# Performance work log

Measured on AMD Instinct MI355X. Metric: run time of the kernel, lower is better.

The kernel has to match this reference:

```python
import jax, jax.numpy as jnp
import numpy as np

B, C, H, W = 4, 256, 32, 32
N_HEADS, N_GROUPS = 8, 4
HEAD_C = C // N_HEADS            # 32
GROUP_C = C // N_GROUPS          # 64
GROUP_HEADS = N_HEADS // N_GROUPS  # 2
OFFSET_RANGE_FACTOR = 4.0
SCALE = HEAD_C ** -0.5
EPS = 1e-5


def grid_sample(img, grid):
    """Bilinear grid_sample, align_corners=True, zeros padding.
    img: (N, Ch, Hi, Wi); grid: (N, Hg, Wg, 2) with (x, y) in [-1, 1]."""
    N, Ch, Hi, Wi = img.shape
    x = (grid[..., 0] + 1.0) * 0.5 * (Wi - 1)
    y = (grid[..., 1] + 1.0) * 0.5 * (Hi - 1)
    x0 = jnp.floor(x); y0 = jnp.floor(y)
    x1 = x0 + 1.0; y1 = y0 + 1.0
    wx1 = x - x0; wx0 = 1.0 - wx1
    wy1 = y - y0; wy0 = 1.0 - wy1
    img_flat = img.reshape(N, Ch, Hi * Wi)

    def corner(xi, yi, w):
        valid = (xi >= 0) & (xi <= Wi - 1) & (yi >= 0) & (yi <= Hi - 1)
        xc = jnp.clip(xi, 0, Wi - 1).astype(jnp.int32)
        yc = jnp.clip(yi, 0, Hi - 1).astype(jnp.int32)
        idx = yc * Wi + xc  # (N, Hg, Wg)
        vals = jax.vmap(lambda im, ix: im[:, ix])(img_flat, idx)  # (N, Ch, Hg, Wg)
        return vals * (w * valid)[:, None, :, :]

    return (corner(x0, y0, wx0 * wy0) + corner(x1, y0, wx1 * wy0)
            + corner(x0, y1, wx0 * wy1) + corner(x1, y1, wx1 * wy1))


def setup_inputs() -> dict:
    key = jax.random.key(0)
    ks = jax.random.split(key, 12)
    s = C ** -0.5
    return {
        "q_feat": jax.random.normal(ks[0], (B, C, H, W), jnp.float32),
        "kv_feat": jax.random.normal(ks[1], (B, C, H, W), jnp.float32),
        "Wq": jax.random.normal(ks[2], (C, C), jnp.float32) * s,
        "bq": jnp.zeros((C,), jnp.float32),
        "Wk": jax.random.normal(ks[3], (C, C), jnp.float32) * s,
        "bk": jnp.zeros((C,), jnp.float32),
        "Wv": jax.random.normal(ks[4], (C, C), jnp.float32) * s,
        "bv": jnp.zeros((C,), jnp.float32),
        "Wo": jax.random.normal(ks[5], (C, C), jnp.float32) * s,
        "bo": jnp.zeros((C,), jnp.float32),
        "off_dw_w": jax.random.normal(ks[6], (GROUP_C, 1, 3, 3), jnp.float32) / 3.0,
        "off_dw_b": jnp.zeros((GROUP_C,), jnp.float32),
        "off_ln_w": jnp.ones((GROUP_C,), jnp.float32),
        "off_ln_b": jnp.zeros((GROUP_C,), jnp.float32),
        "off_pw_w": jax.random.normal(ks[7], (2, GROUP_C), jnp.float32) * GROUP_C ** -0.5,
        "rpe_table": jax.random.normal(ks[8], (N_HEADS, 2 * H - 1, 2 * W - 1), jnp.float32) * 0.01,
    }


def reference(q_feat, kv_feat, Wq, bq, Wk, bk, Wv, bv, Wo, bo,
              off_dw_w, off_dw_b, off_ln_w, off_ln_b, off_pw_w, rpe_table):
    Bg = B * N_GROUPS
    n = H * W
    # q projection (1x1 conv)
    q = jnp.einsum('oi,bihw->bohw', Wq, q_feat) + bq[:, None, None]
    # offset network on grouped q
    q_off = q.reshape(Bg, GROUP_C, H, W)
    x = jax.lax.conv_general_dilated(q_off, off_dw_w, (1, 1), ((1, 1), (1, 1)),
                                     feature_group_count=GROUP_C,
                                     dimension_numbers=('NCHW', 'OIHW', 'NCHW'))
    x = x + off_dw_b[:, None, None]
    mu = x.mean(1, keepdims=True)
    var = x.var(1, keepdims=True)
    x = (x - mu) / jnp.sqrt(var + EPS) * off_ln_w[:, None, None] + off_ln_b[:, None, None]
    x = jax.nn.gelu(x, approximate=False)
    offset = jnp.einsum('oc,bchw->bohw', off_pw_w, x)  # (Bg, 2, H, W), (y, x)
    off_range = jnp.array([1.0 / (H - 1), 1.0 / (W - 1)], jnp.float32).reshape(1, 2, 1, 1)
    offset = jnp.tanh(offset) * off_range * OFFSET_RANGE_FACTOR
    offset = offset.transpose(0, 2, 3, 1)  # (Bg, H, W, 2)
    # reference points in [-1, 1]
    ref_y = (jnp.linspace(0.5, H - 0.5, H) / (H - 1.0)) * 2.0 - 1.0
    ref_x = (jnp.linspace(0.5, W - 0.5, W) / (W - 1.0)) * 2.0 - 1.0
    ref = jnp.stack(jnp.meshgrid(ref_y, ref_x, indexing='ij'), -1)  # (H, W, 2)
    pos = offset + ref[None]  # (Bg, H, W, 2), (y, x), no clamp (offset_range_factor >= 0)
    # deformable sampling of kv features
    kv_g = kv_feat.reshape(Bg, GROUP_C, H, W)
    x_sampled = grid_sample(kv_g, pos[..., ::-1]).reshape(B, C, n)
    k = jnp.einsum('oi,bin->bon', Wk, x_sampled) + bk[:, None]
    v = jnp.einsum('oi,bin->bon', Wv, x_sampled) + bv[:, None]
    qf = q.reshape(B, N_HEADS, HEAD_C, n)
    kf = k.reshape(B, N_HEADS, HEAD_C, n)
    vf = v.reshape(B, N_HEADS, HEAD_C, n)
    attn = jnp.einsum('bhcm,bhcn->bhmn', qf, kf) * SCALE
    # relative-position bias via bilinear sampling of rpe table
    gy = (jnp.arange(H, dtype=jnp.float32) / (H - 1.0)) * 2.0 - 1.0
    gx = (jnp.arange(W, dtype=jnp.float32) / (W - 1.0)) * 2.0 - 1.0
    q_grid = jnp.stack(jnp.meshgrid(gy, gx, indexing='ij'), -1).reshape(n, 2)
    pos_flat = pos.reshape(Bg, n, 2)
    disp = (q_grid[None, :, None, :] - pos_flat[:, None, :, :]) * 0.5  # (Bg, m, n, 2)
    rpe = jnp.broadcast_to(
        rpe_table.reshape(1, N_GROUPS, GROUP_HEADS, 2 * H - 1, 2 * W - 1),
        (B, N_GROUPS, GROUP_HEADS, 2 * H - 1, 2 * W - 1)
    ).reshape(Bg, GROUP_HEADS, 2 * H - 1, 2 * W - 1)
    bias = grid_sample(rpe, disp[..., ::-1])  # (Bg, GROUP_HEADS, m, n)
    attn = attn + bias.reshape(B, N_HEADS, n, n)
    attn = jax.nn.softmax(attn, axis=-1)
    out = jnp.einsum('bhmn,bhcn->bhcm', attn, vf).reshape(B, C, H, W)
    out = jnp.einsum('oi,bihw->bohw', Wo, out) + bo[:, None, None]
    return out
```

## Files before the change

### kernel.cpp

```cpp
#include <hip/hip_runtime.h>
#include <hip/hip_bf16.h>
#include <math.h>

#define BB 4
#define CC 256
#define HH 32
#define WW 32
#define NPIX 1024
#define NHEADS 8
#define NGROUPS 4
#define HEADC 32
#define GROUPC 64
#define BG 16
#define RPE_N 3969
#define SCALE_QK 0.17677669529663687f
#define LN_EPS 1e-5f

#define W_Q   0
#define W_POS 1048576
#define W_XS  1081344
#define W_KT  2129920
#define W_VV  2654208
#define W_AO  3178496

using frag  = __attribute__((ext_vector_type(8))) short;
using f32x4 = __attribute__((ext_vector_type(4))) float;

struct InPtrs { const void* p[16]; };

__device__ __forceinline__ float tof(float x){ return x; }
__device__ __forceinline__ float tof(__hip_bfloat16 x){ return __bfloat162float(x); }
__device__ __forceinline__ short bfs(float v) {
  __hip_bfloat16 h = __float2bfloat16(v);
  return *(short*)&h;
}
__device__ __forceinline__ bool is_f32(const void* lnw) {
  return *(const unsigned int*)lnw == 0x3F800000u;
}
__device__ __forceinline__ float ldm(const void* p, size_t i, bool f32m) {
  return f32m ? ((const float*)p)[i] : __bfloat162float(((const __hip_bfloat16*)p)[i]);
}

template<int TM>
__device__ __forceinline__ void gemm_body(const void* xsrc, bool xf32,
    const void* wraw, bool wf32, int b, int o0, int mb,
    short* Bs, f32x4* acc) {
  const int tid = threadIdx.x;
  const int wave = tid >> 6, lane = tid & 63, quad = lane >> 4, l15 = lane & 15;
  const int og = wave & 3, mh = wave >> 2;
  const int MS = TM >> 5;
  const int NE = TM >> 4;

  size_t gbase[NE];
  int lbase[NE];
  #pragma unroll
  for (int it = 0; it < NE; ++it) {
    int i = tid + 512 * it;
    int mm = i & (TM - 1), kk = i / TM;
    gbase[it] = ((size_t)(b * CC + kk)) * NPIX + mb + mm;
    lbase[it] = mm * 72 + ((((kk >> 3) ^ (mm & 3))) << 4) + (kk & 7);
  }

  float v[NE];
  #pragma unroll
  for (int it = 0; it < NE; ++it)
    v[it] = xf32 ? ((const float*)xsrc)[gbase[it]]
                 : __bfloat162float(((const __hip_bfloat16*)xsrc)[gbase[it]]);

  for (int s = 0; s < 8; ++s) {
    short* buf = Bs + (s & 1) * (TM * 72);
    #pragma unroll
    for (int it = 0; it < NE; ++it) {
      __hip_bfloat16 h = __float2bfloat16(v[it]);
      buf[lbase[it]] = *(short*)&h;
      buf[lbase[it] + 8] = bfs(v[it] - __bfloat162float(h));
    }
    if (s < 7) {
      size_t koff = (size_t)(s + 1) * 32 * NPIX;
      #pragma unroll
      for (int it = 0; it < NE; ++it)
        v[it] = xf32 ? ((const float*)xsrc)[gbase[it] + koff]
                     : __bfloat162float(((const __hip_bfloat16*)xsrc)[gbase[it] + koff]);
    }
    const int k0 = s * 32;
    size_t wofs = (size_t)(o0 + og * 16 + l15) * CC + k0 + quad * 8;
    float wv[8];
    if (wf32) {
      float4 wa = *(const float4*)((const float*)wraw + wofs);
      float4 wb = *(const float4*)((const float*)wraw + wofs + 4);
      wv[0]=wa.x; wv[1]=wa.y; wv[2]=wa.z; wv[3]=wa.w;
      wv[4]=wb.x; wv[5]=wb.y; wv[6]=wb.z; wv[7]=wb.w;
    } else {
      const __hip_bfloat16* wp = (const __hip_bfloat16*)wraw + wofs;
      #pragma unroll
      for (int j = 0; j < 8; ++j) wv[j] = __bfloat162float(wp[j]);
    }
    frag wh, wl;
    #pragma unroll
    for (int j = 0; j < 8; ++j) {
      __hip_bfloat16 h = __float2bfloat16(wv[j]);
      wh[j] = *(short*)&h;
      wl[j] = bfs(wv[j] - __bfloat162float(h));
    }
    __syncthreads();
    #pragma unroll
    for (int ms = 0; ms < MS; ++ms) {
      int ml = mh * (TM >> 1) + ms * 16 + l15;
      const short* bp = buf + ml * 72 + ((quad ^ (ml & 3)) << 4);
      frag bh = *(const frag*)bp;
      frag bl = *(const frag*)(bp + 8);
      acc[ms] = __builtin_amdgcn_mfma_f32_16x16x32_bf16(wh, bh, acc[ms], 0, 0, 0);
      acc[ms] = __builtin_amdgcn_mfma_f32_16x16x32_bf16(wh, bl, acc[ms], 0, 0, 0);
      acc[ms] = __builtin_amdgcn_mfma_f32_16x16x32_bf16(wl, bh, acc[ms], 0, 0, 0);
    }
  }
}

__global__ __launch_bounds__(512)
void qproj_kernel(InPtrs ip, float* __restrict__ q) {
  __shared__ __align__(16) short Bs[2 * 32 * 72];
  bool f32m = is_f32(ip.p[12]);
  int mb = blockIdx.x * 32, o0 = blockIdx.y * 64, b = blockIdx.z;
  int tid = threadIdx.x;
  int wave = tid >> 6, lane = tid & 63, quad = lane >> 4, l15 = lane & 15;
  f32x4 acc[1] = {{0.f,0.f,0.f,0.f}};
  gemm_body<32>(ip.p[0], f32m, ip.p[2], f32m, b, o0, mb, Bs, acc);
  int og = wave & 3, mh = wave >> 2;
  int od = o0 + og * 16 + quad * 4;
  float bv[4];
  #pragma unroll
  for (int r = 0; r < 4; ++r) bv[r] = ldm(ip.p[3], od + r, f32m);
  int m = mb + mh * 16 + l15;
  #pragma unroll
  for (int r = 0; r < 4; ++r)
    q[(size_t)(b * CC + od + r) * NPIX + m] = acc[0][r] + bv[r];
}

__global__ __launch_bounds__(512)
void kvproj_kernel(InPtrs ip, const float* __restrict__ xs,
                   __hip_bfloat16* __restrict__ kT, __hip_bfloat16* __restrict__ vbf) {
  __shared__ __align__(16) char arena[2 * 64 * 72 * 2];
  bool f32m = is_f32(ip.p[12]);
  int mt = blockIdx.x, ot = blockIdx.y, b = blockIdx.z;
  int mb = mt * 64;
  bool isV = (ot >= 4);
  int o0 = (ot & 3) * 64;
  const void* wraw = isV ? ip.p[6] : ip.p[4];
  const void* braw = isV ? ip.p[7] : ip.p[5];
  int tid = threadIdx.x;
  int wave = tid >> 6, lane = tid & 63, quad = lane >> 4, l15 = lane & 15;
  f32x4 acc[2] = {{0.f,0.f,0.f,0.f},{0.f,0.f,0.f,0.f}};
  gemm_body<64>(xs, true, wraw, f32m, b, o0, mb, (short*)arena, acc);
  int og = wave & 3, mh = wave >> 2;
  int od = o0 + og * 16 + quad * 4;
  float bv[4];
  #pragma unroll
  for (int r = 0; r < 4; ++r) bv[r] = ldm(braw, od + r, f32m);
  if (isV) {
    #pragma unroll
    for (int ms = 0; ms < 2; ++ms) {
      int m = mb + mh * 32 + ms * 16 + l15;
      #pragma unroll
      for (int r = 0; r < 4; ++r)
        vbf[(size_t)(b * CC + od + r) * NPIX + m] = __float2bfloat16(acc[ms][r] + bv[r]);
    }
  } else {
    __syncthreads();
    float* Ds = (float*)arena;
    #pragma unroll
    for (int ms = 0; ms < 2; ++ms) {
      int ml = mh * 32 + ms * 16 + l15;
      #pragma unroll
      for (int r = 0; r < 4; ++r)
        Ds[(og * 16 + quad * 4 + r) * 65 + ml] = acc[ms][r] + bv[r];
    }
    __syncthreads();
    int ot4 = ot & 3;
    {
      int q2 = tid;
      int m = q2 >> 3, cc = q2 & 7;
      __hip_bfloat16 t8[8];
      #pragma unroll
      for (int j = 0; j < 8; ++j)
        t8[j] = __float2bfloat16(Ds[(cc * 8 + j) * 65 + m]);
      int h = ot4 * 2 + (cc >> 2);
      size_t addr = ((size_t)(b * NHEADS + h) * NPIX + mb + m) * HEADC + (cc & 3) * 8;
      *(uint4*)((short*)kT + addr) = *(const uint4*)t8;
    }
  }
}

__global__ __launch_bounds__(512)
void oproj_kernel(InPtrs ip, const float* __restrict__ ao, void* __restrict__ out) {
  __shared__ __align__(16) short Bs[2 * 32 * 72];
  bool f32m = is_f32(ip.p[12]);
  int mb = blockIdx.x * 32, o0 = blockIdx.y * 64, b = blockIdx.z;
  int tid = threadIdx.x;
  int wave = tid >> 6, lane = tid & 63, quad = lane >> 4, l15 = lane & 15;
  f32x4 acc[1] = {{0.f,0.f,0.f,0.f}};
  gemm_body<32>(ao, true, ip.p[8], f32m, b, o0, mb, Bs, acc);
  int og = wave & 3, mh = wave >> 2;
  int od = o0 + og * 16 + quad * 4;
  float bv[4];
  #pragma unroll
  for (int r = 0; r < 4; ++r) bv[r] = ldm(ip.p[9], od + r, f32m);
  int m = mb + mh * 16 + l15;
  #pragma unroll
  for (int r = 0; r < 4; ++r) {
    float val = acc[0][r] + bv[r];
    size_t idx = (size_t)(b * CC + od + r) * NPIX + m;
    if (f32m) ((float*)out)[idx] = val;
    else      ((__hip_bfloat16*)out)[idx] = __float2bfloat16(val);
  }
}

template<typename T>
__device__ __forceinline__ float tap4(const T* __restrict__ img,
                                      int x0, int y0,
                                      float wx0, float wx1, float wy0, float wy1) {
  bool xv0 = (x0 >= 0) & (x0 < WW);
  bool xv1 = (x0 >= -1) & (x0 < WW - 1);
  bool yv0 = (y0 >= 0) & (y0 < HH);
  bool yv1 = (y0 >= -1) & (y0 < HH - 1);
  float acc = 0.0f;
  if (xv0 & yv0) acc += wx0 * wy0 * tof(img[y0 * WW + x0]);
  if (xv1 & yv0) acc += wx1 * wy0 * tof(img[y0 * WW + x0 + 1]);
  if (xv0 & yv1) acc += wx0 * wy1 * tof(img[(y0 + 1) * WW + x0]);
  if (xv1 & yv1) acc += wx1 * wy1 * tof(img[(y0 + 1) * WW + x0 + 1]);
  return acc;
}

__global__ __launch_bounds__(512)
void offsample_kernel(InPtrs ip, const float* __restrict__ q,
                      float* __restrict__ pos, float* __restrict__ xs) {
  __shared__ float qs[128][65];
  __shared__ float posl[2][64];
  bool f32m = is_f32(ip.p[12]);
  int blk = blockIdx.x;
  int hh2 = blk & 15, bg = blk >> 4;
  int b = bg >> 2, g = bg & 3;
  int tid = threadIdx.x;
  const float* qg = q + (size_t)(b * CC + g * GROUPC) * NPIX;
  #pragma unroll
  for (int k = 0; k < 16; ++k) {
    int idx = tid + 512 * k;
    int ww = idx & 31, c = (idx >> 5) & 63, r3 = idx >> 11;
    int yy = hh2 * 2 - 1 + r3;
    float v = (yy >= 0 && yy < HH) ? qg[(size_t)c * NPIX + yy * WW + ww] : 0.0f;
    qs[r3 * 32 + ww][c] = v;
  }
  __syncthreads();
  {
    int wave = tid >> 6, c = tid & 63;
    int lr = wave >> 2, w4 = wave & 3;
    float wdw[9];
    #pragma unroll
    for (int j = 0; j < 9; ++j) wdw[j] = ldm(ip.p[10], c * 9 + j, f32m);
    float bdw = ldm(ip.p[11], c, f32m);
    float lnw = ldm(ip.p[12], c, f32m), lnb = ldm(ip.p[13], c, f32m);
    float pwy = ldm(ip.p[14], c, f32m), pwx = ldm(ip.p[14], GROUPC + c, f32m);

    for (int p8 = 0; p8 < 8; ++p8) {
      int ww = w4 * 8 + p8;
      float x = bdw;
      #pragma unroll
      for (int dy = 0; dy < 3; ++dy)
        #pragma unroll
        for (int dx = 0; dx < 3; ++dx) {
          int xx = ww + dx - 1;
          if (xx >= 0 && xx < WW) x += wdw[dy * 3 + dx] * qs[(lr + dy) * 32 + xx][c];
        }
      float s = x, s2 = x * x;
      #pragma unroll
      for (int off = 32; off > 0; off >>= 1) {
        s  += __shfl_xor(s,  off);
        s2 += __shfl_xor(s2, off);
      }
      float mu  = s * (1.0f / 64.0f);
      float var = s2 * (1.0f / 64.0f) - mu * mu;
      float xn = (x - mu) * (1.0f / sqrtf(var + LN_EPS)) * lnw + lnb;
      float ge = 0.5f * xn * (1.0f + erff(xn * 0.70710678118654752f));
      float oy = pwy * ge, ox = pwx * ge;
      #pragma unroll
      for (int off = 32; off > 0; off >>= 1) {
        oy += __shfl_xor(oy, off);
        ox += __shfl_xor(ox, off);
      }
      if (c == 0) {
        int hh = hh2 * 2 + lr;
        float fy = tanhf(oy) * (4.0f / 31.0f);
        float fx = tanhf(ox) * (4.0f / 31.0f);
        float ry = ((0.5f + (float)hh) / 31.0f) * 2.0f - 1.0f;
        float rx = ((0.5f + (float)ww) / 31.0f) * 2.0f - 1.0f;
        float py = fy + ry, px = fx + rx;
        int m = hh * 32 + ww;
        pos[((size_t)bg * NPIX + m) * 2 + 0] = py;
        pos[((size_t)bg * NPIX + m) * 2 + 1] = px;
        posl[lr][ww * 2 + 0] = py;
        posl[lr][ww * 2 + 1] = px;
      }
    }
  }
  __syncthreads();
  #pragma unroll
  for (int k = 0; k < 8; ++k) {
    int s = tid + 512 * k;
    int ww = s & 31, lr = (s >> 5) & 1, c = s >> 6;
    float py = posl[lr][ww * 2 + 0], px = posl[lr][ww * 2 + 1];
    float xi = (px + 1.0f) * 15.5f, yi = (py + 1.0f) * 15.5f;
    float x0f = floorf(xi), y0f = floorf(yi);
    float wx1 = xi - x0f, wx0 = 1.0f - wx1;
    float wy1 = yi - y0f, wy0 = 1.0f - wy1;
    int x0 = (int)x0f, y0 = (int)y0f;
    size_t img_off = (size_t)(b * CC + g * GROUPC + c) * NPIX;
    float acc;
    if (f32m) acc = tap4((const float*)ip.p[1] + img_off, x0, y0, wx0, wx1, wy0, wy1);
    else      acc = tap4((const __hip_bfloat16*)ip.p[1] + img_off, x0, y0, wx0, wx1, wy0, wy1);
    xs[img_off + (hh2 * 2 + lr) * 32 + ww] = acc;
  }
}

__global__ __launch_bounds__(512)
void attn_mfma_kernel(InPtrs ip, const float* __restrict__ q,
                      const __hip_bfloat16* __restrict__ kT,
                      const __hip_bfloat16* __restrict__ vbf,
                      const float* __restrict__ pos, float* __restrict__ ao) {
  __shared__ __align__(16) __hip_bfloat16 Pl[16][1032];
  __shared__ float rpes[RPE_N];
  __shared__ __align__(16) __hip_bfloat16 qA[4][16][40];
  __shared__ float redmax[8 * 16];
  __shared__ float redsum[8 * 16];

  bool f32m = is_f32(ip.p[12]);
  int bh = blockIdx.x;
  int b = bh >> 3, h = bh & 7;
  int m0base = blockIdx.y * 64;
  int tid = threadIdx.x;
  int bg = b * 4 + (h >> 1);

  size_t slice = (size_t)(b * CC + h * HEADC) * NPIX;
  const short* kTb = (const short*)kT + (size_t)bh * NPIX * HEADC;
  const short* vb = (const short*)vbf + slice;
  const float* qb = q + slice;
  const float* posb = pos + (size_t)bg * NPIX * 2;

  for (int i = tid; i < RPE_N; i += 512)
    rpes[i] = ldm(ip.p[15], (size_t)h * RPE_N + i, f32m);
  #pragma unroll
  for (int e = 0; e < 4; ++e) {
    int idx = tid + 512 * e;
    int t = idx >> 9, j = idx & 511;
    int r = j & 15, c = j >> 4;
    qA[t][r][c] = __float2bfloat16(qb[(size_t)c * NPIX + m0base + t * 16 + r] * SCALE_QK);
  }
  __syncthreads();

  int wave = tid >> 6, lane = tid & 63;
  int quad = lane >> 4, l15 = lane & 15;
  int nbase = wave * 128;

  for (int t = 0; t < 4; ++t) {
    int m0 = m0base + t * 16;
    if (t) __syncthreads();

    frag aq = *(const frag*)&qA[t][l15][quad * 8];
    float qgy = (float)(m0 >> 5) * (2.0f / 31.0f) - 1.0f;
    float ybase = 31.0f + 15.5f * qgy;
    float qgx0 = (float)(m0 & 31) * (2.0f / 31.0f) - 1.0f;
    float xbase0 = 31.0f + 15.5f * qgx0;

    float sreg[8][4];
    #pragma unroll
    for (int t8 = 0; t8 < 8; ++t8) {
      int n = nbase + t8 * 16 + l15;
      frag bk = *(const frag*)(kTb + (size_t)n * HEADC + quad * 8);
      f32x4 d = __builtin_amdgcn_mfma_f32_16x16x32_bf16(aq, bk, (f32x4){0.f,0.f,0.f,0.f}, 0, 0, 0);
      float2 pp = *(const float2*)(posb + 2 * n);
      float yi = ybase - 15.5f * pp.x;
      float y0f = floorf(yi);
      int y0 = (int)y0f;
      float wy1 = yi - y0f, wy0 = 1.0f - wy1;
      bool yv0 = (y0 >= 0) & (y0 < 63);
      bool yv1 = (y0 >= -1) & (y0 < 62);
      int row0 = y0 * 63;
      float xi0 = xbase0 - 15.5f * pp.y;
      float x0f = floorf(xi0);
      int x0 = (int)x0f;
      float wx1 = xi0 - x0f, wx0 = 1.0f - wx1;
      float u[5];
      #pragma unroll
      for (int jj = 0; jj < 5; ++jj) {
        int xj = x0 + quad * 4 + jj;
        bool xv = (xj >= 0) & (xj < 63);
        int a = row0 + xj;
        int a0c = min(max(a, 0), RPE_N - 1);
        int a1c = min(max(a + 63, 0), RPE_N - 1);
        float t0 = (yv0 & xv) ? rpes[a0c] : 0.0f;
        float t1 = (yv1 & xv) ? rpes[a1c] : 0.0f;
        u[jj] = wy0 * t0 + wy1 * t1;
      }
      #pragma unroll
      for (int reg = 0; reg < 4; ++reg)
        sreg[t8][reg] = d[reg] + wx0 * u[reg] + wx1 * u[reg + 1];
    }

    float ps[4], pm[4];
    #pragma unroll
    for (int reg = 0; reg < 4; ++reg) {
      float m = sreg[0][reg];
      #pragma unroll
      for (int t8 = 1; t8 < 8; ++t8) m = fmaxf(m, sreg[t8][reg]);
      m = fmaxf(m, __shfl_xor(m, 1));
      m = fmaxf(m, __shfl_xor(m, 2));
      m = fmaxf(m, __shfl_xor(m, 4));
      m = fmaxf(m, __shfl_xor(m, 8));
      pm[reg] = m;
      ps[reg] = 0.0f;
    }
    #pragma unroll
    for (int t8 = 0; t8 < 8; ++t8) {
      int n = nbase + t8 * 16 + l15;
      #pragma unroll
      for (int reg = 0; reg < 4; ++reg) {
        float p = __expf(sreg[t8][reg] - pm[reg]);
        Pl[quad * 4 + reg][n] = __float2bfloat16(p);
        ps[reg] += p;
      }
    }
    #pragma unroll
    for (int reg = 0; reg < 4; ++reg) {
      ps[reg] += __shfl_xor(ps[reg], 1);
      ps[reg] += __shfl_xor(ps[reg], 2);
      ps[reg] += __shfl_xor(ps[reg], 4);
      ps[reg] += __shfl_xor(ps[reg], 8);
    }
    if (l15 == 0) {
      #pragma unroll
      for (int reg = 0; reg < 4; ++reg) {
        redmax[wave * 16 + quad * 4 + reg] = pm[reg];
        redsum[wave * 16 + quad * 4 + reg] = ps[reg];
      }
    }

    f32x4 acc0 = {0.f,0.f,0.f,0.f}, acc1 = {0.f,0.f,0.f,0.f};
    #pragma unroll
    for (int ks = 0; ks < 4; ++ks) {
      int koff = nbase + ks * 32 + quad * 8;
      frag ap = *(const frag*)&Pl[l15][koff];
      frag bv0 = *(const frag*)(vb + (size_t)l15 * NPIX + koff);
      frag bv1 = *(const frag*)(vb + (size_t)(16 + l15) * NPIX + koff);
      acc0 = __builtin_amdgcn_mfma_f32_16x16x32_bf16(ap, bv0, acc0, 0, 0, 0);
      acc1 = __builtin_amdgcn_mfma_f32_16x16x32_bf16(ap, bv1, acc1, 0, 0, 0);
    }
    __syncthreads();

    float* part = (float*)&Pl[0][0];
    {
      int e0 = (0 * 16 + l15) * 16 + quad * 4;
      int e1 = (1 * 16 + l15) * 16 + quad * 4;
      #pragma unroll
      for (int reg = 0; reg < 4; ++reg) {
        part[wave * 512 + e0 + reg] = acc0[reg];
        part[wave * 512 + e1 + reg] = acc1[reg];
      }
    }
    __syncthreads();

    {
      int c = tid >> 4, r = tid & 15;
      float M = -1e30f;
      #pragma unroll
      for (int w2 = 0; w2 < 8; ++w2) M = fmaxf(M, redmax[w2 * 16 + r]);
      float num = 0.0f, den = 0.0f;
      #pragma unroll
      for (int w2 = 0; w2 < 8; ++w2) {
        float sc = __expf(redmax[w2 * 16 + r] - M);
        num += part[w2 * 512 + tid] * sc;
        den += redsum[w2 * 16 + r] * sc;
      }
      ao[slice + (size_t)c * NPIX + m0 + r] = num / den;
    }
  }
}

extern "C" void kernel_launch(void* const* d_in, const int* in_sizes, int n_in,
                              void* d_out, int out_size, void* d_ws, size_t ws_size,
                              hipStream_t stream) {
  float* ws  = (float*)d_ws;
  float* q   = ws + W_Q;
  float* pos = ws + W_POS;
  float* xs  = ws + W_XS;
  __hip_bfloat16* kT  = (__hip_bfloat16*)(ws + W_KT);
  __hip_bfloat16* vbf = (__hip_bfloat16*)(ws + W_VV);
  float* ao  = ws + W_AO;

  InPtrs ip;
  for (int i = 0; i < 16; ++i) ip.p[i] = d_in[i];

  qproj_kernel<<<dim3(32, 4, 4), 512, 0, stream>>>(ip, q);
  offsample_kernel<<<BG * 16, 512, 0, stream>>>(ip, q, pos, xs);
  kvproj_kernel<<<dim3(16, 8, 4), 512, 0, stream>>>(ip, xs, kT, vbf);
  attn_mfma_kernel<<<dim3(32, 16), 512, 0, stream>>>(ip, q, kT, vbf, pos, ao);
  oproj_kernel<<<dim3(32, 4, 4), 512, 0, stream>>>(ip, ao, d_out);
}
```

Baseline: 195.2 us.

## Pack padded bf16 pair table for rpe bias lookups in attention kernel

Replaces the fp32 rpe table in shared memory with a zero-padded 70x71 table of packed bf16 pairs (value at x and x+1). Each bias lookup then needs six 32-bit LDS reads with no bounds checks or clamping, instead of ten predicated reads with index arithmetic. The launch bounds also request 4 blocks per CU. Storing the rpe values as bf16 lowers bias precision. The padding assumes sampled coordinates stay within a 4-cell margin, so values further out would read out of range instead of returning zero.

```diff
diff --git a/kernel.cpp b/kernel.cpp
--- a/kernel.cpp
+++ b/kernel.cpp
@@ -1,6 +1,7 @@
 #include <hip/hip_runtime.h>
 #include <hip/hip_bf16.h>
 #include <math.h>
+#include <stdint.h>
 
 #define BB 4
 #define CC 256
@@ -40,6 +41,8 @@
 __device__ __forceinline__ float ldm(const void* p, size_t i, bool f32m) {
   return f32m ? ((const float*)p)[i] : __bfloat162float(((const __hip_bfloat16*)p)[i]);
 }
+__device__ __forceinline__ float lof(uint32_t g){ return __uint_as_float(g << 16); }
+__device__ __forceinline__ float hif(uint32_t g){ return __uint_as_float(g & 0xffff0000u); }
 
 template<int TM>
 __device__ __forceinline__ void gemm_body(const void* xsrc, bool xf32,
@@ -320,13 +323,13 @@
   }
 }
 
-__global__ __launch_bounds__(512)
+__global__ __launch_bounds__(512, 4)
 void attn_mfma_kernel(InPtrs ip, const float* __restrict__ q,
                       const __hip_bfloat16* __restrict__ kT,
                       const __hip_bfloat16* __restrict__ vbf,
                       const float* __restrict__ pos, float* __restrict__ ao) {
   __shared__ __align__(16) __hip_bfloat16 Pl[16][1032];
-  __shared__ float rpes[RPE_N];
+  __shared__ uint32_t Du[70 * 71];
   __shared__ __align__(16) __hip_bfloat16 qA[4][16][40];
   __shared__ float redmax[8 * 16];
   __shared__ float redsum[8 * 16];
@@ -344,8 +347,18 @@
   const float* qb = q + slice;
   const float* posb = pos + (size_t)bg * NPIX * 2;
 
-  for (int i = tid; i < RPE_N; i += 512)
-    rpes[i] = ldm(ip.p[15], (size_t)h * RPE_N + i, f32m);
+  {
+    const size_t rbase = (size_t)h * RPE_N;
+    for (int i = tid; i < 70 * 71; i += 512) {
+      int r = i / 71, c = i - r * 71;
+      int y = r - 4, x = c - 4;
+      bool yv = (y >= 0) & (y < 63);
+      float va = (yv & (x >= 0) & (x < 63)) ? ldm(ip.p[15], rbase + y * 63 + x, f32m) : 0.0f;
+      float vb2 = (yv & (x >= -1) & (x < 62)) ? ldm(ip.p[15], rbase + y * 63 + x + 1, f32m) : 0.0f;
+      __hip_bfloat16 ha = __float2bfloat16(va), hb = __float2bfloat16(vb2);
+      Du[i] = (uint32_t)*(unsigned short*)&ha | ((uint32_t)*(unsigned short*)&hb << 16);
+    }
+  }
   #pragma unroll
   for (int e = 0; e < 4; ++e) {
     int idx = tid + 512 * e;
@@ -378,27 +391,21 @@
       float2 pp = *(const float2*)(posb + 2 * n);
       float yi = ybase - 15.5f * pp.x;
       float y0f = floorf(yi);
-      int y0 = (int)y0f;
       float wy1 = yi - y0f, wy0 = 1.0f - wy1;
-      bool yv0 = (y0 >= 0) & (y0 < 63);
-      bool yv1 = (y0 >= -1) & (y0 < 62);
-      int row0 = y0 * 63;
       float xi0 = xbase0 - 15.5f * pp.y;
       float x0f = floorf(xi0);
-      int x0 = (int)x0f;
       float wx1 = xi0 - x0f, wx0 = 1.0f - wx1;
+      int row = (int)y0f + 4;
+      int col = (int)x0f + 4 + quad * 4;
+      const uint32_t* Dp = Du + row * 71 + col;
+      uint32_t g0 = Dp[0],  g1 = Dp[2],  g2 = Dp[4];
+      uint32_t h0 = Dp[71], h1 = Dp[73], h2 = Dp[75];
       float u[5];
-      #pragma unroll
-      for (int jj = 0; jj < 5; ++jj) {
-        int xj = x0 + quad * 4 + jj;
-        bool xv = (xj >= 0) & (xj < 63);
-        int a = row0 + xj;
-        int a0c = min(max(a, 0), RPE_N - 1);
-        int a1c = min(max(a + 63, 0), RPE_N - 1);
-        float t0 = (yv0 & xv) ? rpes[a0c] : 0.0f;
-        float t1 = (yv1 & xv) ? rpes[a1c] : 0.0f;
-        u[jj] = wy0 * t0 + wy1 * t1;
-      }
+      u[0] = wy0 * lof(g0) + wy1 * lof(h0);
+      u[1] = wy0 * hif(g0) + wy1 * hif(h0);
+      u[2] = wy0 * lof(g1) + wy1 * lof(h1);
+      u[3] = wy0 * hif(g1) + wy1 * hif(h1);
+      u[4] = wy0 * lof(g2) + wy1 * lof(h2);
       #pragma unroll
       for (int reg = 0; reg < 4; ++reg)
         sreg[t8][reg] = d[reg] + wx0 * u[reg] + wx1 * u[reg + 1];
```

New measurement: 185.1 us. -5.2%, faster.
